# Kernel tuning notes

Measured on AMD Instinct MI355X. Metric: run time of the kernel, lower is better.

## Reference

```python
import jax, jax.numpy as jnp
import numpy as np

BN_EPS = 1e-5
LEAKY_SLOPE = 0.2


def setup_inputs() -> dict:
    key = jax.random.key(0)
    k1, k2 = jax.random.split(key, 2)
    B, C, N, O = 8, 64, 4096, 64
    data = jax.random.normal(k1, (B, C, N), dtype=jnp.float32)
    # 1x1 Conv2d(channels_in=2C, channels_out=O, bias=False) kernel -> [O, 2C]
    W = jax.random.normal(k2, (O, 2 * C), dtype=jnp.float32) * 0.05
    gamma = jnp.ones((O,), dtype=jnp.float32)
    beta = jnp.zeros((O,), dtype=jnp.float32)
    return {"data": data, "W": W, "gamma": gamma, "beta": beta, "k": 20}


def reference(data, W, gamma, beta, k):
    B, C, N = data.shape
    xt = jnp.transpose(data, (0, 2, 1))                 # [B, N, C]
    # knn via -||xi - xj||^2 = -xx - 2*(-x.x) - xx  (topk of negative sq dist)
    inner = -2.0 * jnp.matmul(xt, data)                 # [B, N, N]
    xx = jnp.sum(data * data, axis=1)                   # [B, N]
    pdist = -xx[:, :, None] - inner - xx[:, None, :]    # [B, N, N]
    idx = jax.lax.top_k(pdist, k)[1]                    # [B, N, k] int32
    # gather neighbor features: [B, N, k, C]
    feat = jax.vmap(lambda d, i: d[i])(xt, idx)
    center = xt[:, :, None, :]                          # [B, N, 1, C]
    edge = jnp.concatenate(
        [feat - center, jnp.broadcast_to(center, (B, N, k, C))], axis=-1
    )                                                   # [B, N, k, 2C]
    # 1x1 conv == channel matmul -> [B, O, N, k]
    y = jnp.einsum('bnkc,oc->bonk', edge, W)
    # BatchNorm2d, training-mode batch stats over (B, N, k) per channel
    mean = jnp.mean(y, axis=(0, 2, 3), keepdims=True)
    var = jnp.mean((y - mean) ** 2, axis=(0, 2, 3), keepdims=True)
    y = (y - mean) * jax.lax.rsqrt(var + BN_EPS)
    y = y * gamma[None, :, None, None] + beta[None, :, None, None]
    # LeakyReLU(0.2)
    y = jnp.where(y >= 0, y, LEAKY_SLOPE * y)
    # max over k neighbors -> [B, O, N]
    return jnp.max(y, axis=-1)
```

## Files before the change

kernel.cpp:

```cpp
#include <hip/hip_runtime.h>
#include <hip/hip_fp16.h>
#include <float.h>

#define B 8
#define C 64
#define N 4096
#define O 64
#define KMAX 32
#define NREP 64

typedef unsigned short u16;
typedef unsigned int u32;
typedef unsigned long long u64;
typedef __attribute__((ext_vector_type(8))) u16 u16x8;
typedef __attribute__((ext_vector_type(8))) short bf16x8;
typedef __attribute__((ext_vector_type(4))) float f32x4;

__device__ __forceinline__ u16 f2bf(float f) {
    unsigned u = __builtin_bit_cast(unsigned, f);
    unsigned r = (u + 0x7FFFu + ((u >> 16) & 1)) >> 16;
    return (u16)r;
}

__global__ __launch_bounds__(256) void ec_prep(const float* __restrict__ x,
                                               const float* __restrict__ W,
                                               float* __restrict__ xx,
                                               float* __restrict__ xt,
                                               u16* __restrict__ xtb,
                                               __half* __restrict__ u,
                                               __half* __restrict__ v) {
    __shared__ float xs[64][65];
    __shared__ float W1[C][64];
    __shared__ float Wd[C][64];
    __shared__ float rs[4][64];
    const int blk = blockIdx.x;
    const int b = blk >> 6;
    const int n0 = (blk & 63) << 6;
    const int t = threadIdx.x;
#pragma unroll
    for (int p = 0; p < 16; ++p) {
        int q = t + 256 * p; int c = q >> 6, j = q & 63;
        xs[c][j] = x[(size_t)b * C * N + (size_t)c * N + n0 + j];
    }
#pragma unroll
    for (int p = 0; p < 16; ++p) {
        int q = t + 256 * p; int c = q >> 6, o = q & 63;
        float w1 = W[o * 128 + c];
        float w2 = W[o * 128 + 64 + c];
        W1[c][o] = w1; Wd[c][o] = w2 - w1;
    }
    __syncthreads();
    {
        const int j = t >> 2, g = t & 3;
        float vals[16]; float ss = 0.f;
#pragma unroll
        for (int i = 0; i < 16; ++i) { float f = xs[g * 16 + i][j]; vals[i] = f; ss += f * f; }
        rs[g][j] = ss;
        size_t rowb = ((size_t)b * N + n0 + j) * 64 + g * 16;
#pragma unroll
        for (int i = 0; i < 4; ++i) {
            float4 v4 = { vals[4 * i], vals[4 * i + 1], vals[4 * i + 2], vals[4 * i + 3] };
            *(float4*)&xt[rowb + 4 * i] = v4;
        }
        u16x8 h0, h1;
#pragma unroll
        for (int i = 0; i < 8; ++i) { h0[i] = f2bf(vals[i]); h1[i] = f2bf(vals[8 + i]); }
        *(u16x8*)&xtb[rowb] = h0;
        *(u16x8*)&xtb[rowb + 8] = h1;
    }
    {
        const int o = t & 63, ji = t >> 6;
        float su[16] = {}, sv[16] = {};
#pragma unroll 1
        for (int c = 0; c < C; ++c) {
            float w1 = W1[c][o];
            float wd = Wd[c][o];
#pragma unroll
            for (int p = 0; p < 16; ++p) {
                float xv = xs[c][ji + 4 * p];
                su[p] = fmaf(xv, w1, su[p]);
                sv[p] = fmaf(xv, wd, sv[p]);
            }
        }
#pragma unroll
        for (int p = 0; p < 16; ++p) {
            size_t base = ((size_t)b * N + n0 + ji + 4 * p) * O + o;
            u[base] = __float2half(su[p]);
            v[base] = __float2half(sv[p]);
        }
    }
    __syncthreads();
    if (t < 64) xx[(size_t)b * N + t + n0] = rs[0][t] + rs[1][t] + rs[2][t] + rs[3][t];
}

#define CXD(a, b) { u32 mx_ = max(a, b); b = min(a, b); a = mx_; }
#define CXA(a, b) { u32 mn_ = min(a, b); b = max(a, b); a = mn_; }
#define BSORT8(e0,e1,e2,e3,e4,e5,e6,e7) { \
    CXD(e0,e1) CXA(e2,e3) CXD(e4,e5) CXA(e6,e7) \
    CXD(e0,e2) CXD(e1,e3) CXA(e4,e6) CXA(e5,e7) \
    CXD(e0,e1) CXD(e2,e3) CXA(e4,e5) CXA(e6,e7) \
    CXD(e0,e4) CXD(e1,e5) CXD(e2,e6) CXD(e3,e7) \
    CXD(e0,e2) CXD(e1,e3) CXD(e4,e6) CXD(e5,e7) \
    CXD(e0,e1) CXD(e2,e3) CXD(e4,e5) CXD(e6,e7) }
#define MERGETOP8(t0,t1,t2,t3,t4,t5,t6,t7, e0,e1,e2,e3,e4,e5,e6,e7) { \
    t0 = max(t0, e7); t1 = max(t1, e6); t2 = max(t2, e5); t3 = max(t3, e4); \
    t4 = max(t4, e3); t5 = max(t5, e2); t6 = max(t6, e1); t7 = max(t7, e0); \
    CXD(t0,t4) CXD(t1,t5) CXD(t2,t6) CXD(t3,t7) \
    CXD(t0,t2) CXD(t1,t3) CXD(t4,t6) CXD(t5,t7) \
    CXD(t0,t1) CXD(t2,t3) CXD(t4,t5) CXD(t6,t7) }

__global__ __launch_bounds__(256) void ec_gemm(const u16* __restrict__ xtb,
                                               const float* __restrict__ xx,
                                               u32* __restrict__ cand) {
    __shared__ u16 lds[18432 + 8];
    const int t = threadIdx.x;
    const int m0 = blockIdx.x * 128, n0 = blockIdx.y * 128;
    const int b = blockIdx.z;
    const u16* xa = xtb + (size_t)b * N * 64;
#pragma unroll
    for (int p = 0; p < 4; ++p) {
        int q = t + 256 * p;
        int row = q >> 3, ch = q & 7;
        int by = (row * 128 + ch * 16) ^ ((row & 7) << 4);
        *(u16x8*)((char*)lds + by) = *(const u16x8*)&xa[(size_t)(n0 + row) * 64 + ch * 8];
        *(u16x8*)((char*)lds + 16384 + by) = *(const u16x8*)&xa[(size_t)(m0 + row) * 64 + ch * 8];
    }
    __syncthreads();
    const int w = t >> 6, lane = t & 63;
    const int wr = w >> 1, wc = w & 1;
    const int fr = lane & 15, fg = lane >> 4;
    f32x4 acc[4][4] = {};
#pragma unroll
    for (int ks = 0; ks < 2; ++ks) {
        bf16x8 af[4], bg[4];
#pragma unroll
        for (int fi = 0; fi < 4; ++fi) {
            int rowA = 64 * wr + 16 * fi + fr;
            int byA = (rowA * 128 + ks * 64 + fg * 16) ^ ((rowA & 7) << 4);
            af[fi] = *(const bf16x8*)((const char*)lds + byA);
            int rowB = 64 * wc + 16 * fi + fr;
            int byB = (rowB * 128 + ks * 64 + fg * 16) ^ ((rowB & 7) << 4);
            bg[fi] = *(const bf16x8*)((const char*)lds + 16384 + byB);
        }
#pragma unroll
        for (int fi = 0; fi < 4; ++fi)
#pragma unroll
            for (int fj = 0; fj < 4; ++fj)
                acc[fi][fj] = __builtin_amdgcn_mfma_f32_16x16x32_bf16(af[fi], bg[fj], acc[fi][fj], 0, 0, 0);
    }
    float xmK[4];
#pragma unroll
    for (int fj = 0; fj < 4; ++fj)
        xmK[fj] = 1536.f - xx[(size_t)b * N + m0 + 64 * wc + 16 * fj + fr];
    __syncthreads();
    u16* ep = lds + w * 4608;
#pragma unroll
    for (int fi = 0; fi < 4; ++fi)
#pragma unroll
        for (int fj = 0; fj < 4; ++fj)
#pragma unroll
            for (int r = 0; r < 4; ++r) {
                float dvp = fmaf(2.f, acc[fi][fj][r], xmK[fj]);
                u32 bits = __builtin_bit_cast(u32, dvp);
                int row = 16 * fi + fg * 4 + r, col = 16 * fj + fr;
                ep[row * 72 + col] = (u16)(bits >> 8);
            }
    __syncthreads();
    const u16* myrow = lds + w * 4608 + lane * 72;
    const int mbase = m0 + (wc << 6);
    const u32 invb = (u32)(4095 - mbase);
    u32 t0, t1, t2, t3, t4, t5, t6, t7;
    {
        u16x8 q = *(const u16x8*)&myrow[0];
        t0 = ((u32)q[0] << 12) | (invb - 0); t1 = ((u32)q[1] << 12) | (invb - 1);
        t2 = ((u32)q[2] << 12) | (invb - 2); t3 = ((u32)q[3] << 12) | (invb - 3);
        t4 = ((u32)q[4] << 12) | (invb - 4); t5 = ((u32)q[5] << 12) | (invb - 5);
        t6 = ((u32)q[6] << 12) | (invb - 6); t7 = ((u32)q[7] << 12) | (invb - 7);
        BSORT8(t0, t1, t2, t3, t4, t5, t6, t7)
    }
#pragma unroll
    for (int g = 1; g < 8; ++g) {
        u16x8 q = *(const u16x8*)&myrow[g * 8];
        const u32 inv0 = invb - (u32)(g * 8);
        u32 e0 = ((u32)q[0] << 12) | (inv0 - 0), e1 = ((u32)q[1] << 12) | (inv0 - 1);
        u32 e2 = ((u32)q[2] << 12) | (inv0 - 2), e3 = ((u32)q[3] << 12) | (inv0 - 3);
        u32 e4 = ((u32)q[4] << 12) | (inv0 - 4), e5 = ((u32)q[5] << 12) | (inv0 - 5);
        u32 e6 = ((u32)q[6] << 12) | (inv0 - 6), e7 = ((u32)q[7] << 12) | (inv0 - 7);
        BSORT8(e0, e1, e2, e3, e4, e5, e6, e7)
        MERGETOP8(t0, t1, t2, t3, t4, t5, t6, t7, e0, e1, e2, e3, e4, e5, e6, e7)
    }
    const int row_g = n0 + 64 * wr + lane;
    u32* cp = cand + (((size_t)b * N + row_g) * 64 + (size_t)(blockIdx.x * 2 + wc)) * 8;
    uint4 w0 = { t0, t1, t2, t3 }, w1 = { t4, t5, t6, t7 };
    *(uint4*)cp = w0;
    *(uint4*)(cp + 4) = w1;
}

#define CXI(i, j) { u32 mn_ = min(c[i], c[j]); c[i] = max(c[i], c[j]); c[j] = mn_; }
#define CLEAN8() { CXI(0,4) CXI(1,5) CXI(2,6) CXI(3,7) \
                   CXI(0,2) CXI(1,3) CXI(4,6) CXI(5,7) \
                   CXI(0,1) CXI(2,3) CXI(4,5) CXI(6,7) }
#define CLEAN32(lane) { \
    u32 pr_[8]; \
    _Pragma("unroll") for (int i_ = 0; i_ < 8; ++i_) pr_[i_] = __shfl_xor(c[i_], 2); \
    { bool km_ = ((lane) & 2) == 0; \
      _Pragma("unroll") for (int i_ = 0; i_ < 8; ++i_) \
          c[i_] = km_ ? max(c[i_], pr_[i_]) : min(c[i_], pr_[i_]); } \
    _Pragma("unroll") for (int i_ = 0; i_ < 8; ++i_) pr_[i_] = __shfl_xor(c[i_], 1); \
    { bool km_ = ((lane) & 1) == 0; \
      _Pragma("unroll") for (int i_ = 0; i_ < 8; ++i_) \
          c[i_] = km_ ? max(c[i_], pr_[i_]) : min(c[i_], pr_[i_]); } \
    CLEAN8() }

__global__ __launch_bounds__(256) void ec_sel(const u32* __restrict__ cand,
                                              const float* __restrict__ xt,
                                              const float* __restrict__ xx,
                                              const __half* __restrict__ u,
                                              const __half* __restrict__ v,
                                              const int* __restrict__ kptr,
                                              __half2* __restrict__ ext,
                                              float* __restrict__ statsR) {
    __shared__ float sxn[4][64];
    __shared__ int scand[4][32];
    __shared__ float rsum[256], rsum2[256];
    const int t = threadIdx.x, w = t >> 6, lane = t & 63;
    const int b = blockIdx.y;
    const int n = blockIdx.x * 4 + w;
    const int k = *kptr;

    const u32* cp = cand + (((size_t)b * N + n) * 64 + lane) * 8;
    uint4 a0 = *(const uint4*)cp, a1 = *(const uint4*)(cp + 4);
    u32 c[8] = { a0.x, a0.y, a0.z, a0.w, a1.x, a1.y, a1.z, a1.w };

    {
        u32 pr[8];
#pragma unroll
        for (int i = 0; i < 8; ++i) pr[i] = __shfl_xor(c[7 - i], 1);
        bool lo = (lane & 1) == 0;
#pragma unroll
        for (int i = 0; i < 8; ++i) {
            u32 mx = max(c[i], pr[i]), mn = min(c[i], pr[i]);
            c[i] = lo ? mx : mn;
        }
        CLEAN8()
    }
    {
        u32 pr[8];
#pragma unroll
        for (int i = 0; i < 8; ++i) pr[i] = __shfl_xor(c[7 - i], 1);
        bool up = (lane & 2) != 0;
#pragma unroll
        for (int i = 0; i < 8; ++i) c[i] = up ? pr[i] : c[i];
        CLEAN32(lane)
    }
#define MERGE_TOP32(mask) { \
        u32 pr[8]; \
        _Pragma("unroll") for (int i = 0; i < 8; ++i) pr[i] = __shfl_xor(c[7 - i], mask); \
        _Pragma("unroll") for (int i = 0; i < 8; ++i) c[i] = max(c[i], pr[i]); \
        CLEAN32(lane) }
    MERGE_TOP32(7)
    MERGE_TOP32(11)
    MERGE_TOP32(19)
    MERGE_TOP32(35)
#undef MERGE_TOP32

    if (lane < 4) {
        int base = lane * 8;
#pragma unroll
        for (int i = 0; i < 8; ++i) scand[w][base + i] = 4095 - (int)(c[i] & 0xFFFu);
    }
    sxn[w][lane] = xt[((size_t)b * N + n) * 64 + lane];
    __syncthreads();

    const float* xt_ = xt + (size_t)b * N * 64;
    const int jc = lane & 31, h = lane >> 5;
    const int mj = scand[w][jc];
    const float* xr = xt_ + (size_t)mj * 64 + h * 32;
    float acc = 0.f;
#pragma unroll
    for (int q8 = 0; q8 < 8; ++q8) {
        float4 g4 = *(const float4*)&xr[q8 * 4];
        float4 xn4 = *(const float4*)&sxn[w][h * 32 + q8 * 4];
        acc += g4.x * xn4.x + g4.y * xn4.y + g4.z * xn4.z + g4.w * xn4.w;
    }
    acc += __shfl_xor(acc, 32);
    float ex = 2.f * acc - xx[(size_t)b * N + mj];
    unsigned fu = __builtin_bit_cast(unsigned, ex);
    unsigned sf = fu ^ (unsigned)(((int)fu >> 31) | 0x80000000);
    u64 key = ((u64)sf << 12) | (u64)(4095 - mj);
    if (h) key = 0;

#pragma unroll
    for (int ls = 1; ls <= 5; ++ls) {
        const int s = 1 << ls;
        const bool lb = (lane & s) == 0;
#pragma unroll
        for (int dd = s >> 1; dd >= 1; dd >>= 1) {
            const bool km = ((lane & dd) == 0) == lb;
            u64 pv = __shfl_xor(key, dd);
            u64 mn = key < pv ? key : pv;
            u64 mx = key < pv ? pv : key;
            key = km ? mx : mn;
        }
    }
    int m_final = 4095 - (int)(key & 0xFFFu);

    const __half* ub = u + (size_t)b * N * O;
    size_t rowb = (size_t)b * N + n;
    float vv = __half2float(v[rowb * O + lane]);
    float gmax = -FLT_MAX, gmin = FLT_MAX, gs = 0.f, gs2 = 0.f;
    if (k == 20) {
        int mks[20];
#pragma unroll
        for (int kk = 0; kk < 20; ++kk) mks[kk] = __shfl(m_final, kk);
        float g[20];
#pragma unroll
        for (int kk = 0; kk < 20; ++kk)
            g[kk] = __half2float(ub[(size_t)mks[kk] * O + lane]);
#pragma unroll
        for (int kk = 0; kk < 20; ++kk) {
            gs += g[kk]; gs2 += g[kk] * g[kk];
            gmax = fmaxf(gmax, g[kk]); gmin = fminf(gmin, g[kk]);
        }
    } else {
        int mks[KMAX];
#pragma unroll
        for (int kk = 0; kk < KMAX; ++kk) mks[kk] = __shfl(m_final, kk);
        float g[KMAX];
#pragma unroll
        for (int kk = 0; kk < KMAX; ++kk)
            g[kk] = __half2float(ub[(size_t)mks[kk] * O + lane]);
#pragma unroll
        for (int kk = 0; kk < KMAX; ++kk) {
            if (kk < k) {
                gs += g[kk]; gs2 += g[kk] * g[kk];
                gmax = fmaxf(gmax, g[kk]); gmin = fminf(gmin, g[kk]);
            }
        }
    }
    float fk = (float)k;
    float s  = gs + fk * vv;
    float s2 = gs2 + 2.f * vv * gs + fk * vv * vv;
    ext[rowb * O + lane] = __halves2half2(__float2half(gmax + vv), __float2half(gmin + vv));
    rsum[t] = s; rsum2[t] = s2;
    __syncthreads();
    if (t < 64) {
        float a  = rsum[t] + rsum[t + 64] + rsum[t + 128] + rsum[t + 192];
        float a2 = rsum2[t] + rsum2[t + 64] + rsum2[t + 128] + rsum2[t + 192];
        float* sr = statsR + (size_t)(blockIdx.x & (NREP - 1)) * 128;
        atomicAdd(&sr[t], a);
        atomicAdd(&sr[64 + t], a2);
    }
}

__global__ void ec_final(const float* __restrict__ statsR,
                         const float* __restrict__ gamma,
                         const float* __restrict__ beta,
                         const int* __restrict__ kptr,
                         float* __restrict__ scsh) {
    int o = threadIdx.x;
    int k = *kptr;
    float s = 0.f, s2 = 0.f;
    for (int r = 0; r < NREP; ++r) {
        s  += statsR[r * 128 + o];
        s2 += statsR[r * 128 + 64 + o];
    }
    float M = (float)B * (float)N * (float)k;
    float mean = s / M;
    float var = s2 / M - mean * mean;
    var = fmaxf(var, 0.f);
    float sc = gamma[o] * rsqrtf(var + 1e-5f);
    float sh = beta[o] - mean * sc;
    scsh[o] = sc;
    scsh[64 + o] = sh;
}

__global__ __launch_bounds__(256) void ec_out(const __half2* __restrict__ ext,
                                              const float* __restrict__ scsh,
                                              float* __restrict__ out) {
    __shared__ float res[64][65];
    const int blk = blockIdx.x;
    const int b = blk >> 6;
    const int n0 = (blk & 63) << 6;
    const int t = threadIdx.x;
    {
        const int o = t & 63, ni = t >> 6;
        float sc = scsh[o], sh = scsh[64 + o];
#pragma unroll 1
        for (int p = 0; p < 16; ++p) {
            int nl = ni * 16 + p;
            size_t a = ((size_t)b * N + n0 + nl) * O + o;
            __half2 e = ext[a];
            float y = (sc >= 0.f) ? __low2float(e) : __high2float(e);
            float z = sc * y + sh;
            res[nl][o] = (z >= 0.f) ? z : 0.2f * z;
        }
    }
    __syncthreads();
    {
        const int j = t & 63, oi = t >> 6;
#pragma unroll 1
        for (int p = 0; p < 16; ++p) {
            int o2 = oi * 16 + p;
            out[(size_t)b * O * N + (size_t)o2 * N + n0 + j] = res[j][o2];
        }
    }
}

extern "C" void kernel_launch(void* const* d_in, const int* in_sizes, int n_in,
                              void* d_out, int out_size, void* d_ws, size_t ws_size,
                              hipStream_t stream) {
    const float* x     = (const float*)d_in[0];
    const float* W     = (const float*)d_in[1];
    const float* gamma = (const float*)d_in[2];
    const float* beta  = (const float*)d_in[3];
    const int*   kptr  = (const int*)d_in[4];
    float* out = (float*)d_out;

    char* ws = (char*)d_ws;
    u32*    cand = (u32*)ws;    ws += (size_t)B * N * 64 * 8 * 4;
    float*  xx   = (float*)ws;  ws += (size_t)B * N * 4;
    float*  xt   = (float*)ws;  ws += (size_t)B * N * C * 4;
    u16*    xtb  = (u16*)ws;    ws += (size_t)B * N * C * 2;
    __half* u_t  = (__half*)ws; ws += (size_t)B * N * O * 2;
    __half* v_t  = (__half*)ws; ws += (size_t)B * N * O * 2;
    __half2* ext = (__half2*)ws; ws += (size_t)B * N * O * 4;
    float* statsR = (float*)ws; ws += (size_t)NREP * 128 * 4;
    float* scsh  = (float*)ws;

    hipMemsetAsync(statsR, 0, NREP * 128 * 4, stream);
    ec_prep<<<B * N / 64, 256, 0, stream>>>(x, W, xx, xt, xtb, u_t, v_t);
    ec_gemm<<<dim3(N / 128, N / 128, B), 256, 0, stream>>>(xtb, xx, cand);
    ec_sel<<<dim3(N / 4, B), 256, 0, stream>>>(cand, xt, xx, u_t, v_t, kptr, ext, statsR);
    ec_final<<<1, 64, 0, stream>>>(statsR, gamma, beta, kptr, scsh);
    ec_out<<<B * N / 64, 256, 0, stream>>>(ext, scsh, out);
}
```

Before: 172.1 us.

## Merge per-wave top-8 candidates in LDS before writing, halving candidate traffic

The GEMM kernel now merges the two column-half waves' top-8 lists through LDS, so each block writes one top-8 list per row instead of two. This halves the candidate buffer written to global memory and read back by the selection kernel. The selection kernel is rewritten to hold 4 candidates per lane and uses fewer shuffle merge stages. The quantized distance key also moves from a 1536 offset with a shift of 8 to a 2560 offset with a shift of 7, giving the sort key one more bit of precision. In exchange the GEMM kernel pays for extra barriers and a merge step.

```diff
diff --git a/kernel.cpp b/kernel.cpp
--- a/kernel.cpp
+++ b/kernel.cpp
@@ -151,7 +151,7 @@
     float xmK[4];
 #pragma unroll
     for (int fj = 0; fj < 4; ++fj)
-        xmK[fj] = 1536.f - xx[(size_t)b * N + m0 + 64 * wc + 16 * fj + fr];
+        xmK[fj] = 2560.f - xx[(size_t)b * N + m0 + 64 * wc + 16 * fj + fr];
     __syncthreads();
     u16* ep = lds + w * 4608;
 #pragma unroll
@@ -163,7 +163,7 @@
                 float dvp = fmaf(2.f, acc[fi][fj][r], xmK[fj]);
                 u32 bits = __builtin_bit_cast(u32, dvp);
                 int row = 16 * fi + fg * 4 + r, col = 16 * fj + fr;
-                ep[row * 72 + col] = (u16)(bits >> 8);
+                ep[row * 72 + col] = (u16)(bits >> 7);
             }
     __syncthreads();
     const u16* myrow = lds + w * 4608 + lane * 72;
@@ -189,28 +189,37 @@
         BSORT8(e0, e1, e2, e3, e4, e5, e6, e7)
         MERGETOP8(t0, t1, t2, t3, t4, t5, t6, t7, e0, e1, e2, e3, e4, e5, e6, e7)
     }
-    const int row_g = n0 + 64 * wr + lane;
-    u32* cp = cand + (((size_t)b * N + row_g) * 64 + (size_t)(blockIdx.x * 2 + wc)) * 8;
-    uint4 w0 = { t0, t1, t2, t3 }, w1 = { t4, t5, t6, t7 };
-    *(uint4*)cp = w0;
-    *(uint4*)(cp + 4) = w1;
-}
-
-#define CXI(i, j) { u32 mn_ = min(c[i], c[j]); c[i] = max(c[i], c[j]); c[j] = mn_; }
-#define CLEAN8() { CXI(0,4) CXI(1,5) CXI(2,6) CXI(3,7) \
-                   CXI(0,2) CXI(1,3) CXI(4,6) CXI(5,7) \
-                   CXI(0,1) CXI(2,3) CXI(4,5) CXI(6,7) }
-#define CLEAN32(lane) { \
-    u32 pr_[8]; \
-    _Pragma("unroll") for (int i_ = 0; i_ < 8; ++i_) pr_[i_] = __shfl_xor(c[i_], 2); \
-    { bool km_ = ((lane) & 2) == 0; \
-      _Pragma("unroll") for (int i_ = 0; i_ < 8; ++i_) \
-          c[i_] = km_ ? max(c[i_], pr_[i_]) : min(c[i_], pr_[i_]); } \
-    _Pragma("unroll") for (int i_ = 0; i_ < 8; ++i_) pr_[i_] = __shfl_xor(c[i_], 1); \
-    { bool km_ = ((lane) & 1) == 0; \
-      _Pragma("unroll") for (int i_ = 0; i_ < 8; ++i_) \
-          c[i_] = km_ ? max(c[i_], pr_[i_]) : min(c[i_], pr_[i_]); } \
-    CLEAN8() }
+    __syncthreads();
+    u32* mbuf = (u32*)lds;
+    if (wc) {
+        u32* mp = mbuf + (size_t)((wr << 6) | lane) * 8;
+        uint4 w0 = { t0, t1, t2, t3 }, w1 = { t4, t5, t6, t7 };
+        *(uint4*)mp = w0;
+        *(uint4*)(mp + 4) = w1;
+    }
+    __syncthreads();
+    if (!wc) {
+        const u32* mp = mbuf + (size_t)((wr << 6) | lane) * 8;
+        uint4 b0 = *(const uint4*)mp, b1 = *(const uint4*)(mp + 4);
+        u32 e0 = b0.x, e1 = b0.y, e2 = b0.z, e3 = b0.w;
+        u32 e4 = b1.x, e5 = b1.y, e6 = b1.z, e7 = b1.w;
+        MERGETOP8(t0, t1, t2, t3, t4, t5, t6, t7, e0, e1, e2, e3, e4, e5, e6, e7)
+        const int row_g = n0 + 64 * wr + lane;
+        u32* cp = cand + (((size_t)b * N + row_g) * 32 + blockIdx.x) * 8;
+        uint4 w0 = { t0, t1, t2, t3 }, w1 = { t4, t5, t6, t7 };
+        *(uint4*)cp = w0;
+        *(uint4*)(cp + 4) = w1;
+    }
+}
+
+#define CX4(i, j) { u32 mn_ = min(c[i], c[j]); c[i] = max(c[i], c[j]); c[j] = mn_; }
+#define CLEAN4IN() { CX4(0,2) CX4(1,3) CX4(0,1) CX4(2,3) }
+#define DSTEP(xorm, bit) { \
+    u32 pr_[4]; \
+    _Pragma("unroll") for (int i_ = 0; i_ < 4; ++i_) pr_[i_] = __shfl_xor(c[i_], xorm); \
+    bool km_ = (lane & (bit)) == 0; \
+    _Pragma("unroll") for (int i_ = 0; i_ < 4; ++i_) \
+        c[i_] = km_ ? max(c[i_], pr_[i_]) : min(c[i_], pr_[i_]); }
 
 __global__ __launch_bounds__(256) void ec_sel(const u32* __restrict__ cand,
                                               const float* __restrict__ xt,
@@ -228,46 +237,49 @@
     const int n = blockIdx.x * 4 + w;
     const int k = *kptr;
 
-    const u32* cp = cand + (((size_t)b * N + n) * 64 + lane) * 8;
-    uint4 a0 = *(const uint4*)cp, a1 = *(const uint4*)(cp + 4);
-    u32 c[8] = { a0.x, a0.y, a0.z, a0.w, a1.x, a1.y, a1.z, a1.w };
-
-    {
-        u32 pr[8];
-#pragma unroll
-        for (int i = 0; i < 8; ++i) pr[i] = __shfl_xor(c[7 - i], 1);
-        bool lo = (lane & 1) == 0;
-#pragma unroll
-        for (int i = 0; i < 8; ++i) {
+    const u32* cp = cand + (((size_t)b * N + n) * 32 + (lane >> 1)) * 8 + (lane & 1) * 4;
+    uint4 a0 = *(const uint4*)cp;
+    u32 c[4] = { a0.x, a0.y, a0.z, a0.w };
+
+    {
+        u32 pr[4];
+#pragma unroll
+        for (int i = 0; i < 4; ++i) pr[i] = __shfl_xor(c[3 - i], 3);
+        bool lo = (lane & 2) == 0;
+#pragma unroll
+        for (int i = 0; i < 4; ++i) {
             u32 mx = max(c[i], pr[i]), mn = min(c[i], pr[i]);
             c[i] = lo ? mx : mn;
         }
-        CLEAN8()
-    }
-    {
-        u32 pr[8];
-#pragma unroll
-        for (int i = 0; i < 8; ++i) pr[i] = __shfl_xor(c[7 - i], 1);
-        bool up = (lane & 2) != 0;
-#pragma unroll
-        for (int i = 0; i < 8; ++i) c[i] = up ? pr[i] : c[i];
-        CLEAN32(lane)
-    }
-#define MERGE_TOP32(mask) { \
-        u32 pr[8]; \
-        _Pragma("unroll") for (int i = 0; i < 8; ++i) pr[i] = __shfl_xor(c[7 - i], mask); \
-        _Pragma("unroll") for (int i = 0; i < 8; ++i) c[i] = max(c[i], pr[i]); \
-        CLEAN32(lane) }
-    MERGE_TOP32(7)
-    MERGE_TOP32(11)
-    MERGE_TOP32(19)
-    MERGE_TOP32(35)
-#undef MERGE_TOP32
-
-    if (lane < 4) {
-        int base = lane * 8;
-#pragma unroll
-        for (int i = 0; i < 8; ++i) scand[w][base + i] = 4095 - (int)(c[i] & 0xFFFu);
+        DSTEP(1, 1)
+        CLEAN4IN()
+    }
+    {
+        u32 pr[4];
+#pragma unroll
+        for (int i = 0; i < 4; ++i) pr[i] = __shfl_xor(c[3 - i], 7);
+        bool lo = (lane & 4) == 0;
+#pragma unroll
+        for (int i = 0; i < 4; ++i) {
+            u32 mx = max(c[i], pr[i]), mn = min(c[i], pr[i]);
+            c[i] = lo ? mx : mn;
+        }
+        DSTEP(2, 2) DSTEP(1, 1)
+        CLEAN4IN()
+    }
+#define MT32(mask) { \
+        u32 pr_[4]; \
+        _Pragma("unroll") for (int i_ = 0; i_ < 4; ++i_) pr_[i_] = __shfl_xor(c[3 - i_], mask); \
+        _Pragma("unroll") for (int i_ = 0; i_ < 4; ++i_) c[i_] = max(c[i_], pr_[i_]); \
+        DSTEP(4, 4) DSTEP(2, 2) DSTEP(1, 1) CLEAN4IN() }
+    MT32(15)
+    MT32(23)
+    MT32(39)
+#undef MT32
+
+    if (lane < 8) {
+#pragma unroll
+        for (int i = 0; i < 4; ++i) scand[w][lane * 4 + i] = 4095 - (int)(c[i] & 0xFFFu);
     }
     sxn[w][lane] = xt[((size_t)b * N + n) * 64 + lane];
     __syncthreads();
@@ -418,7 +430,7 @@
     float* out = (float*)d_out;
 
     char* ws = (char*)d_ws;
-    u32*    cand = (u32*)ws;    ws += (size_t)B * N * 64 * 8 * 4;
+    u32*    cand = (u32*)ws;    ws += (size_t)B * N * 32 * 8 * 4;
     float*  xx   = (float*)ws;  ws += (size_t)B * N * 4;
     float*  xt   = (float*)ws;  ws += (size_t)B * N * C * 4;
     u16*    xtb  = (u16*)ws;    ws += (size_t)B * N * C * 2;
```

Result: faster. 157.3 us (-8.6%).
